# Kernel optimization log

Hardware: AMD Instinct MI355X
Metric: run time of the kernel (lower is better)

## Reference

```python
import jax, jax.numpy as jnp
import numpy as np
import math

B, C, D, H, W = 8, 128, 64, 32, 32
SHRINK = C // 2  # 64
EPS = 1e-5


def setup_inputs() -> dict:
    key = jax.random.key(0)
    ks = jax.random.split(key, 7)
    x = jax.random.normal(ks[0], (B, C, D, H, W), dtype=jnp.float32)
    # 1x1x1 Conv3d weights collapse to [out_ch, in_ch] matrices (no bias)
    def kaiming(k, shape):
        fan_in = shape[1]
        return jax.random.normal(k, shape, dtype=jnp.float32) * np.float32(math.sqrt(2.0 / fan_in))
    Wk = kaiming(ks[1], (SHRINK, C))
    Wq = kaiming(ks[2], (SHRINK, C))
    Wv = kaiming(ks[3], (SHRINK, C))
    Wo = kaiming(ks[4], (C, SHRINK))
    gamma = jnp.ones((C,), dtype=jnp.float32)
    beta = jnp.zeros((C,), dtype=jnp.float32)
    return {"x": x, "Wk": Wk, "Wq": Wq, "Wv": Wv, "Wo": Wo, "gamma": gamma, "beta": beta}


def reference(x, Wk, Wq, Wv, Wo, gamma, beta):
    b, c, d, h, w = x.shape
    s = Wk.shape[0]
    # BatchNorm3d (training mode: batch statistics over B, D, H, W)
    mean = jnp.mean(x, axis=(0, 2, 3, 4), keepdims=True)
    var = jnp.var(x, axis=(0, 2, 3, 4), keepdims=True)
    xn = (x - mean) * jax.lax.rsqrt(var + EPS)
    xn = xn * gamma[None, :, None, None, None] + beta[None, :, None, None, None]
    # fold spatial into batch: [B*H*W, C, D]
    xr = jnp.transpose(xn, (0, 3, 4, 1, 2)).reshape(b * h * w, c, d)
    k = jnp.einsum('sc,ncd->nsd', Wk, xr)  # [N, S, D]
    q = jnp.einsum('sc,ncd->nsd', Wq, xr)
    v = jnp.einsum('sc,ncd->nsd', Wv, xr)
    scores = jnp.einsum('nsi,nsj->nij', k, q) / jnp.float32(math.sqrt(s))  # [N, D, D]
    a = jax.nn.softmax(scores, axis=1)  # softmax over key-time axis (dim=1)
    attn = jnp.einsum('nsi,nij->nsj', v, a)  # [N, S, D]
    attn = attn.reshape(b, h, w, s, d)
    out = jnp.einsum('os,bhwsd->bodhw', Wo, attn)  # 1x1x1 conv out proj
    return x + out
```

## Files before the change

kernel.cpp:

```cpp
#include <hip/hip_runtime.h>

typedef __attribute__((ext_vector_type(8))) short short8;
typedef __attribute__((ext_vector_type(4))) float f32x4;
typedef unsigned short u16;
typedef unsigned int u32;

#define CNT_PER_C (8*64*32*32)

#define WS_PART  0
#define WS_SCALE 8192
#define WS_SHIFT 8704
#define WS_BIAS  9216
#define WS_WKQV  10240
#define WS_WO    59392
#define WS_OUTP  131072

__device__ __forceinline__ u16 f2bf(float f){
  u32 u = __builtin_bit_cast(u32, f);
  u32 r = u + 0x7FFFu + ((u >> 16) & 1u);
  return (u16)(r >> 16);
}
__device__ __forceinline__ float bf2f(u16 h){
  u32 u = ((u32)h) << 16;
  return __builtin_bit_cast(float, u);
}
__device__ __forceinline__ u32 pk2(float a, float b){
  return (u32)f2bf(a) | ((u32)f2bf(b) << 16);
}

__global__ void k_zero(float* part){
  part[blockIdx.x*256 + threadIdx.x] = 0.f;
}

__global__ __launch_bounds__(256) void k_stats_t(const float* __restrict__ x,
                                                 u16* __restrict__ x_t,
                                                 float* __restrict__ part){
  __shared__ u16 lm[32*512];
  __shared__ float cs[256];
  int t = threadIdx.x;
  cs[t] = 0.f;
  int bid = blockIdx.x;
  int bh = bid>>3, dq = bid&7;
  int b = bh>>5, h = bh&31;
  int d0 = dq*8, n0 = bh*32;
  int s = t>>3, q = t&7;
  float sA=0.f,qA=0.f, sB=0.f,qB=0.f, sC=0.f,qC=0.f, sD=0.f,qD=0.f;
  __syncthreads();
#pragma unroll
  for (int h2=0; h2<2; h2++){
    int w4 = q*4;
#pragma unroll
    for (int i=0;i<16;i++){
      int rowpos = i*32 + s;
      int cl = rowpos & 63, dd = rowpos >> 6;
      int c = h2*64 + cl;
      float4 v = *(const float4*)(x + ((size_t)((b*128 + c)*64 + d0 + dd))*1024 + h*32 + w4);
      float lsum = v.x+v.y+v.z+v.w;
      float lsq  = v.x*v.x+v.y*v.y+v.z*v.z+v.w*v.w;
      if (h2==0){ if ((i&1)==0){ sA+=lsum; qA+=lsq; } else { sB+=lsum; qB+=lsq; } }
      else      { if ((i&1)==0){ sC+=lsum; qC+=lsq; } else { sD+=lsum; qD+=lsq; } }
      lm[(w4+0)*512 + (rowpos ^ ((w4+0)&28))] = f2bf(v.x);
      lm[(w4+1)*512 + (rowpos ^ ((w4+1)&28))] = f2bf(v.y);
      lm[(w4+2)*512 + (rowpos ^ ((w4+2)&28))] = f2bf(v.z);
      lm[(w4+3)*512 + (rowpos ^ ((w4+3)&28))] = f2bf(v.w);
    }
    __syncthreads();
    {
      int n = s, oct = q;
      int oq = oct ^ ((n>>3)&3);
      bool swp = (n & 4) != 0;
#pragma unroll
      for (int m=0;m<8;m++){
        uint4 raw = *(const uint4*)&lm[n*512 + m*64 + oq*8];
        if (swp){ u32 tx=raw.x, ty=raw.y; raw.x=raw.z; raw.y=raw.w; raw.z=tx; raw.w=ty; }
        *(uint4*)(x_t + (size_t)(n0+n)*8192 + (size_t)(d0+m)*128 + h2*64 + oct*8) = raw;
      }
    }
    __syncthreads();
  }
  atomicAdd(&cs[(s    )*2+0], sA); atomicAdd(&cs[(s    )*2+1], qA);
  atomicAdd(&cs[(s+32 )*2+0], sB); atomicAdd(&cs[(s+32 )*2+1], qB);
  atomicAdd(&cs[(s+64 )*2+0], sC); atomicAdd(&cs[(s+64 )*2+1], qC);
  atomicAdd(&cs[(s+96 )*2+0], sD); atomicAdd(&cs[(s+96 )*2+1], qD);
  __syncthreads();
  atomicAdd(&part[(bid&7)*256 + t], cs[t]);
}

__global__ void k_stats2(const float* part, const float* gamma, const float* beta,
                         float* scale, float* shift){
  int c = threadIdx.x;
  float S=0.f, S2=0.f;
  for (int i=0;i<8;i++){ S += part[i*256 + c*2]; S2 += part[i*256 + c*2 + 1]; }
  float inv = 1.0f/(float)CNT_PER_C;
  float mean = S*inv;
  float var  = S2*inv - mean*mean;
  float rstd = rsqrtf(var + 1e-5f);
  float sc = gamma[c]*rstd;
  scale[c] = sc; shift[c] = beta[c] - mean*sc;
}

__global__ __launch_bounds__(256) void k_wprep(const float* wk, const float* wq, const float* wv,
                                               const float* wo, const float* scale,
                                               const float* shift, u16* wkqv_bf, u16* wo_bf,
                                               float* bias){
  int t = threadIdx.x;
  if (t < 192){
    const float* src = (t<64) ? (wk + t*128) : (t<128) ? (wq + (t-64)*128) : (wv + (t-128)*128);
    float bsum = 0.f;
    for (int c=0;c<128;c++){
      float w = src[c];
      bsum += w*shift[c];
      wkqv_bf[t*128+c] = f2bf(w*scale[c]);
    }
    bias[t] = bsum;
  }
  for (int j=t; j<8192; j+=256) wo_bf[j] = f2bf(wo[j]);
}

__global__ __launch_bounds__(256, 2) void k_attn(const u16* __restrict__ x_t,
                                                 const u16* __restrict__ wkqv,
                                                 const u16* __restrict__ wo,
                                                 const float* __restrict__ bias,
                                                 u16* __restrict__ out_pre){
  __shared__ alignas(16) char smb[65536];
  const int t = threadIdx.x, lane = t & 63, wid = t >> 6;
  const int lr = lane & 15, lk = lane >> 4;
  const int n = blockIdx.x*4 + wid;
  char* slot = smb + wid*16384;
  char* lo = slot;
  char* hi = slot + 8192;
  const u16* xg = x_t + (size_t)n*8192;

  short8 xbf[4][4];
#pragma unroll
  for (int ct=0; ct<4; ct++)
#pragma unroll
    for (int ks=0; ks<4; ks++)
      xbf[ct][ks] = *(const short8*)(xg + (ct*16+lr)*128 + ks*32 + lk*8);

#pragma unroll
  for (int mt=0; mt<4; mt++){
    short8 af[4];
#pragma unroll
    for (int ks=0; ks<4; ks++)
      af[ks] = *(const short8*)(wkqv + (size_t)(mt*16 + lr)*128 + ks*32 + lk*8);
    float4 bk4 = *(const float4*)(bias + mt*16 + lk*4);
#pragma unroll
    for (int ct=0; ct<4; ct++){
      f32x4 a = (f32x4){0.f,0.f,0.f,0.f};
#pragma unroll
      for (int ks=0; ks<4; ks++)
        a = __builtin_amdgcn_mfma_f32_16x16x32_bf16(af[ks], xbf[ct][ks], a, 0,0,0);
      a[0]+=bk4.x; a[1]+=bk4.y; a[2]+=bk4.z; a[3]+=bk4.w;
      int d = ct*16 + lr;
      *(uint2*)(lo + d*128 + ((mt*32 + lk*8) ^ ((d&7)<<4))) =
        (uint2){pk2(a[0],a[1]), pk2(a[2],a[3])};
    }
  }
#pragma unroll
  for (int mt=0; mt<4; mt++){
    short8 af[4];
#pragma unroll
    for (int ks=0; ks<4; ks++)
      af[ks] = *(const short8*)(wkqv + (size_t)((mt+4)*16 + lr)*128 + ks*32 + lk*8);
    float4 bq4 = *(const float4*)(bias + 64 + mt*16 + lk*4);
#pragma unroll
    for (int ct=0; ct<4; ct++){
      f32x4 a = (f32x4){0.f,0.f,0.f,0.f};
#pragma unroll
      for (int ks=0; ks<4; ks++)
        a = __builtin_amdgcn_mfma_f32_16x16x32_bf16(af[ks], xbf[ct][ks], a, 0,0,0);
      a[0]+=bq4.x; a[1]+=bq4.y; a[2]+=bq4.z; a[3]+=bq4.w;
      int d = ct*16 + lr;
      *(uint2*)(hi + d*128 + ((mt*32 + lk*8) ^ ((d&7)<<4))) =
        (uint2){pk2(a[0],a[1]), pk2(a[2],a[3])};
    }
  }
  f32x4 vacc[4][4];
#pragma unroll
  for (int mt=0; mt<4; mt++){
    short8 af[4];
#pragma unroll
    for (int ks=0; ks<4; ks++)
      af[ks] = *(const short8*)(wkqv + (size_t)((mt+8)*16 + lr)*128 + ks*32 + lk*8);
    float4 bv4 = *(const float4*)(bias + 128 + mt*16 + lk*4);
#pragma unroll
    for (int ct=0; ct<4; ct++) vacc[mt][ct] = (f32x4){0.f,0.f,0.f,0.f};
#pragma unroll
    for (int ct=0; ct<4; ct++){
#pragma unroll
      for (int ks=0; ks<4; ks++)
        vacc[mt][ct] = __builtin_amdgcn_mfma_f32_16x16x32_bf16(af[ks], xbf[ct][ks], vacc[mt][ct], 0,0,0);
      vacc[mt][ct][0]+=bv4.x; vacc[mt][ct][1]+=bv4.y;
      vacc[mt][ct][2]+=bv4.z; vacc[mt][ct][3]+=bv4.w;
    }
  }

  short8 ka[4][2];
#pragma unroll
  for (int it=0; it<4; it++)
#pragma unroll
    for (int ks2=0; ks2<2; ks2++){
      int i = it*16 + lr;
      ka[it][ks2] = *(const short8*)(lo + i*128 + ((ks2*64 + lk*16) ^ ((i&7)<<4)));
    }
#pragma unroll
  for (int m4=0; m4<4; m4++)
#pragma unroll
    for (int ct=0; ct<4; ct++)
#pragma unroll
      for (int e=0; e<4; e++){
        int sp = m4*16 + lk*4 + e, i = ct*16 + lr;
        *(u16*)(lo + sp*128 + ((i*2) ^ ((sp&7)<<4))) = f2bf(vacc[m4][ct][e]);
      }
  short8 qb[4][2];
#pragma unroll
  for (int jt=0; jt<4; jt++)
#pragma unroll
    for (int ks2=0; ks2<2; ks2++){
      int j = jt*16 + lr;
      qb[jt][ks2] = *(const short8*)(hi + j*128 + ((ks2*64 + lk*16) ^ ((j&7)<<4)));
    }
  f32x4 sc4[4][4];
#pragma unroll
  for (int it=0; it<4; it++)
#pragma unroll
    for (int jt=0; jt<4; jt++) sc4[it][jt] = (f32x4){0.f,0.f,0.f,0.f};
#pragma unroll
  for (int it=0; it<4; it++)
#pragma unroll
    for (int jt=0; jt<4; jt++)
#pragma unroll
      for (int ks2=0; ks2<2; ks2++)
        sc4[it][jt] = __builtin_amdgcn_mfma_f32_16x16x32_bf16(ka[it][ks2], qb[jt][ks2], sc4[it][jt], 0,0,0);

#pragma unroll
  for (int jt=0; jt<4; jt++){
    float m = -1e30f;
#pragma unroll
    for (int it=0; it<4; it++)
#pragma unroll
      for (int e=0; e<4; e++) m = fmaxf(m, sc4[it][jt][e]);
    m = fmaxf(m, __shfl_xor(m, 16, 64));
    m = fmaxf(m, __shfl_xor(m, 32, 64));
    float ssum = 0.f;
#pragma unroll
    for (int it=0; it<4; it++)
#pragma unroll
      for (int e=0; e<4; e++){
        float p = __expf((sc4[it][jt][e] - m) * 0.125f);
        sc4[it][jt][e] = p; ssum += p;
      }
    ssum += __shfl_xor(ssum, 16, 64);
    ssum += __shfl_xor(ssum, 32, 64);
    float inv = 1.0f / ssum;
    int j = jt*16 + lr;
#pragma unroll
    for (int it=0; it<4; it++){
      *(uint2*)(hi + j*128 + ((it*32 + lk*8) ^ ((j&7)<<4))) =
        (uint2){pk2(sc4[it][jt][0]*inv, sc4[it][jt][1]*inv),
                pk2(sc4[it][jt][2]*inv, sc4[it][jt][3]*inv)};
    }
  }

  short8 va[4][2], ab[4][2];
#pragma unroll
  for (int st=0; st<4; st++)
#pragma unroll
    for (int ks2=0; ks2<2; ks2++){
      int s2 = st*16 + lr;
      va[st][ks2] = *(const short8*)(lo + s2*128 + ((ks2*64 + lk*16) ^ ((s2&7)<<4)));
    }
#pragma unroll
  for (int jt=0; jt<4; jt++)
#pragma unroll
    for (int ks2=0; ks2<2; ks2++){
      int j = jt*16 + lr;
      ab[jt][ks2] = *(const short8*)(hi + j*128 + ((ks2*64 + lk*16) ^ ((j&7)<<4)));
    }
  f32x4 at4[4][4];
#pragma unroll
  for (int st=0; st<4; st++)
#pragma unroll
    for (int jt=0; jt<4; jt++) at4[st][jt] = (f32x4){0.f,0.f,0.f,0.f};
#pragma unroll
  for (int st=0; st<4; st++)
#pragma unroll
    for (int jt=0; jt<4; jt++)
#pragma unroll
      for (int ks2=0; ks2<2; ks2++)
        at4[st][jt] = __builtin_amdgcn_mfma_f32_16x16x32_bf16(va[st][ks2], ab[jt][ks2], at4[st][jt], 0,0,0);
#pragma unroll
  for (int st=0; st<4; st++)
#pragma unroll
    for (int jt=0; jt<4; jt++){
      int d = jt*16 + lr;
      *(uint2*)(lo + d*128 + ((st*32 + lk*8) ^ ((d&7)<<4))) =
        (uint2){pk2(at4[st][jt][0], at4[st][jt][1]), pk2(at4[st][jt][2], at4[st][jt][3])};
    }

  short8 tb[4][2];
#pragma unroll
  for (int dt=0; dt<4; dt++)
#pragma unroll
    for (int ks2=0; ks2<2; ks2++){
      int d = dt*16 + lr;
      tb[dt][ks2] = *(const short8*)(lo + d*128 + ((ks2*64 + lk*16) ^ ((d&7)<<4)));
    }
#pragma unroll
  for (int mt=0; mt<8; mt++){
    short8 wa[2];
#pragma unroll
    for (int ks2=0; ks2<2; ks2++)
      wa[ks2] = *(const short8*)(wo + (size_t)(mt*16 + lr)*64 + ks2*32 + lk*8);
    f32x4 oa[4];
#pragma unroll
    for (int dt=0; dt<4; dt++) oa[dt] = (f32x4){0.f,0.f,0.f,0.f};
#pragma unroll
    for (int dt=0; dt<4; dt++)
#pragma unroll
      for (int ks2=0; ks2<2; ks2++)
        oa[dt] = __builtin_amdgcn_mfma_f32_16x16x32_bf16(wa[ks2], tb[dt][ks2], oa[dt], 0,0,0);
#pragma unroll
    for (int dt=0; dt<4; dt++){
      ushort4 xv = *(const ushort4*)(xg + (size_t)(dt*16+lr)*128 + mt*16 + lk*4);
      oa[dt][0] += bf2f(xv.x);
      oa[dt][1] += bf2f(xv.y);
      oa[dt][2] += bf2f(xv.z);
      oa[dt][3] += bf2f(xv.w);
    }
#pragma unroll
    for (int dt=0; dt<4; dt++)
#pragma unroll
      for (int e=0; e<4; e++){
        int cc = mt*16 + lk*4 + e, d = dt*16 + lr;
        *(u16*)(slot + cc*128 + ((d*2) ^ ((cc&7)<<4))) = f2bf(oa[dt][e]);
      }
  }

  u16* og = out_pre + (size_t)n*8192;
#pragma unroll
  for (int r=0;r<16;r++){
    int j = r*64 + lane;
    int cc = j>>3, o = j&7;
    uint4 v = *(const uint4*)(slot + cc*128 + ((o*16) ^ ((cc&7)<<4)));
    *(uint4*)(og + j*8) = v;
  }
}

__global__ __launch_bounds__(256) void k_merge(const u16* out_pre, float* out){
  __shared__ u16 lm[32*512];
  int t = threadIdx.x;
  int bid = blockIdx.x;
  int bh = bid>>2, cq = bid&3;
  int b = bh>>5, h = bh&31;
  int n0 = bh*32;
  int cbase = cq*32;
  int s = t>>3, q = t&7;
  for (int cc=0; cc<4; cc++){
    int cb = cbase + cc*8;
    {
      int n = s;
      int oq = q ^ ((n>>3)&3);
      bool swp = (n & 4) != 0;
#pragma unroll
      for (int i=0;i<8;i++){
        uint4 raw = *(const uint4*)(out_pre + (size_t)(n0+n)*8192 + (cb+i)*64 + q*8);
        if (swp){ u32 tx=raw.x, ty=raw.y; raw.x=raw.z; raw.y=raw.w; raw.z=tx; raw.w=ty; }
        *(uint4*)&lm[n*512 + i*64 + oq*8] = raw;
      }
    }
    __syncthreads();
    {
      int w4 = q*4;
#pragma unroll
      for (int g=0; g<16; g++){
        int row = g*32 + s;
        int ci = row>>6, d = row&63;
        size_t gi = ((size_t)((b*128 + cb + ci)*64 + d))*1024 + h*32 + w4;
        float4 ov;
        ov.x = bf2f(lm[(w4+0)*512 + (row ^ ((w4+0)&28))]);
        ov.y = bf2f(lm[(w4+1)*512 + (row ^ ((w4+1)&28))]);
        ov.z = bf2f(lm[(w4+2)*512 + (row ^ ((w4+2)&28))]);
        ov.w = bf2f(lm[(w4+3)*512 + (row ^ ((w4+3)&28))]);
        *(float4*)(out + gi) = ov;
      }
    }
    __syncthreads();
  }
}

extern "C" void kernel_launch(void* const* d_in, const int* in_sizes, int n_in,
                              void* d_out, int out_size, void* d_ws, size_t ws_size,
                              hipStream_t stream){
  const float* x     = (const float*)d_in[0];
  const float* Wk    = (const float*)d_in[1];
  const float* Wq    = (const float*)d_in[2];
  const float* Wv    = (const float*)d_in[3];
  const float* Wo    = (const float*)d_in[4];
  const float* gamma = (const float*)d_in[5];
  const float* beta  = (const float*)d_in[6];
  float* out = (float*)d_out;
  char* ws = (char*)d_ws;

  float* part  = (float*)(ws + WS_PART);
  float* scale = (float*)(ws + WS_SCALE);
  float* shift = (float*)(ws + WS_SHIFT);
  float* bias  = (float*)(ws + WS_BIAS);
  u16* wkqv  = (u16*)(ws + WS_WKQV);
  u16* wo_bf = (u16*)(ws + WS_WO);
  u16* outp  = (u16*)(ws + WS_OUTP);
  u16* x_t   = (u16*)d_out;

  k_zero   <<<8,    256, 0, stream>>>(part);
  k_stats_t<<<2048, 256, 0, stream>>>(x, x_t, part);
  k_stats2 <<<1,    128, 0, stream>>>(part, gamma, beta, scale, shift);
  k_wprep  <<<1,    256, 0, stream>>>(Wk, Wq, Wv, Wo, scale, shift, wkqv, wo_bf, bias);
  k_attn   <<<2048, 256, 0, stream>>>(x_t, wkqv, wo_bf, bias, outp);
  k_merge  <<<1024, 256, 0, stream>>>(outp, out);
}
```

Baseline: 328.0 us.

## Fuse output transpose into attention kernel and merge stats/weight-prep kernels

The attention kernel now writes fp32 output directly to the final NCDHW layout. Blocks are remapped so that each block's four waves cover four consecutive w positions of the same (b,h), which lets each thread store a float4 along w. This removes the bf16 out_pre intermediate and the separate k_merge transpose kernel, saving a full round trip through global memory. k_stats2 and k_wprep are also merged into one kernel that keeps scale and shift in shared memory, cutting one launch. The stores are now 16-byte chunks strided by 4 KB rather than coalesced rows, and x_t moves from the output buffer into the workspace.

After: 407.5 us. +24.2%, slower.

```diff
diff --git a/kernel.cpp b/kernel.cpp
--- a/kernel.cpp
+++ b/kernel.cpp
@@ -8,12 +8,10 @@
 #define CNT_PER_C (8*64*32*32)
 
 #define WS_PART  0
-#define WS_SCALE 8192
-#define WS_SHIFT 8704
 #define WS_BIAS  9216
 #define WS_WKQV  10240
 #define WS_WO    59392
-#define WS_OUTP  131072
+#define WS_XT    131072
 
 __device__ __forceinline__ u16 f2bf(float f){
   u32 u = __builtin_bit_cast(u32, f);
@@ -86,46 +84,50 @@
   atomicAdd(&part[(bid&7)*256 + t], cs[t]);
 }
 
-__global__ void k_stats2(const float* part, const float* gamma, const float* beta,
-                         float* scale, float* shift){
-  int c = threadIdx.x;
-  float S=0.f, S2=0.f;
-  for (int i=0;i<8;i++){ S += part[i*256 + c*2]; S2 += part[i*256 + c*2 + 1]; }
-  float inv = 1.0f/(float)CNT_PER_C;
-  float mean = S*inv;
-  float var  = S2*inv - mean*mean;
-  float rstd = rsqrtf(var + 1e-5f);
-  float sc = gamma[c]*rstd;
-  scale[c] = sc; shift[c] = beta[c] - mean*sc;
-}
-
-__global__ __launch_bounds__(256) void k_wprep(const float* wk, const float* wq, const float* wv,
-                                               const float* wo, const float* scale,
-                                               const float* shift, u16* wkqv_bf, u16* wo_bf,
-                                               float* bias){
+__global__ __launch_bounds__(256) void k_finalize(const float* part, const float* gamma,
+                                                  const float* beta, const float* wk,
+                                                  const float* wq, const float* wv,
+                                                  const float* wo, u16* wkqv_bf, u16* wo_bf,
+                                                  float* bias){
+  __shared__ float lsc[128], lsh[128];
   int t = threadIdx.x;
+  if (t < 128){
+    float S=0.f, S2=0.f;
+    for (int i=0;i<8;i++){ S += part[i*256 + t*2]; S2 += part[i*256 + t*2 + 1]; }
+    float inv = 1.0f/(float)CNT_PER_C;
+    float mean = S*inv;
+    float var  = S2*inv - mean*mean;
+    float rstd = rsqrtf(var + 1e-5f);
+    float sc = gamma[t]*rstd;
+    lsc[t] = sc; lsh[t] = beta[t] - mean*sc;
+  }
+  __syncthreads();
   if (t < 192){
     const float* src = (t<64) ? (wk + t*128) : (t<128) ? (wq + (t-64)*128) : (wv + (t-128)*128);
     float bsum = 0.f;
     for (int c=0;c<128;c++){
       float w = src[c];
-      bsum += w*shift[c];
-      wkqv_bf[t*128+c] = f2bf(w*scale[c]);
+      bsum += w*lsh[c];
+      wkqv_bf[t*128+c] = f2bf(w*lsc[c]);
     }
     bias[t] = bsum;
   }
   for (int j=t; j<8192; j+=256) wo_bf[j] = f2bf(wo[j]);
 }
 
-__global__ __launch_bounds__(256, 2) void k_attn(const u16* __restrict__ x_t,
-                                                 const u16* __restrict__ wkqv,
-                                                 const u16* __restrict__ wo,
-                                                 const float* __restrict__ bias,
-                                                 u16* __restrict__ out_pre){
+__global__ __launch_bounds__(256, 2) void k_attn_w(const u16* __restrict__ x_t,
+                                                   const u16* __restrict__ wkqv,
+                                                   const u16* __restrict__ wo,
+                                                   const float* __restrict__ bias,
+                                                   float* __restrict__ out){
   __shared__ alignas(16) char smb[65536];
   const int t = threadIdx.x, lane = t & 63, wid = t >> 6;
   const int lr = lane & 15, lk = lane >> 4;
-  const int n = blockIdx.x*4 + wid;
+  const int p = blockIdx.x;
+  const int bh = (p & 7)*32 + (p >> 6);
+  const int wg = (p >> 3) & 7;
+  const int b = bh >> 5, h = bh & 31;
+  const int n = bh*32 + wg*4 + wid;
   char* slot = smb + wid*16384;
   char* lo = slot;
   char* hi = slot + 8192;
@@ -248,8 +250,8 @@
     for (int it=0; it<4; it++)
 #pragma unroll
       for (int e=0; e<4; e++){
-        float p = __expf((sc4[it][jt][e] - m) * 0.125f);
-        sc4[it][jt][e] = p; ssum += p;
+        float pp = __expf((sc4[it][jt][e] - m) * 0.125f);
+        sc4[it][jt][e] = pp; ssum += pp;
       }
     ssum += __shfl_xor(ssum, 16, 64);
     ssum += __shfl_xor(ssum, 32, 64);
@@ -338,55 +340,19 @@
       }
   }
 
-  u16* og = out_pre + (size_t)n*8192;
-#pragma unroll
-  for (int r=0;r<16;r++){
-    int j = r*64 + lane;
-    int cc = j>>3, o = j&7;
-    uint4 v = *(const uint4*)(slot + cc*128 + ((o*16) ^ ((cc&7)<<4)));
-    *(uint4*)(og + j*8) = v;
-  }
-}
-
-__global__ __launch_bounds__(256) void k_merge(const u16* out_pre, float* out){
-  __shared__ u16 lm[32*512];
-  int t = threadIdx.x;
-  int bid = blockIdx.x;
-  int bh = bid>>2, cq = bid&3;
-  int b = bh>>5, h = bh&31;
-  int n0 = bh*32;
-  int cbase = cq*32;
-  int s = t>>3, q = t&7;
-  for (int cc=0; cc<4; cc++){
-    int cb = cbase + cc*8;
-    {
-      int n = s;
-      int oq = q ^ ((n>>3)&3);
-      bool swp = (n & 4) != 0;
-#pragma unroll
-      for (int i=0;i<8;i++){
-        uint4 raw = *(const uint4*)(out_pre + (size_t)(n0+n)*8192 + (cb+i)*64 + q*8);
-        if (swp){ u32 tx=raw.x, ty=raw.y; raw.x=raw.z; raw.y=raw.w; raw.z=tx; raw.w=ty; }
-        *(uint4*)&lm[n*512 + i*64 + oq*8] = raw;
-      }
-    }
-    __syncthreads();
-    {
-      int w4 = q*4;
-#pragma unroll
-      for (int g=0; g<16; g++){
-        int row = g*32 + s;
-        int ci = row>>6, d = row&63;
-        size_t gi = ((size_t)((b*128 + cb + ci)*64 + d))*1024 + h*32 + w4;
-        float4 ov;
-        ov.x = bf2f(lm[(w4+0)*512 + (row ^ ((w4+0)&28))]);
-        ov.y = bf2f(lm[(w4+1)*512 + (row ^ ((w4+1)&28))]);
-        ov.z = bf2f(lm[(w4+2)*512 + (row ^ ((w4+2)&28))]);
-        ov.w = bf2f(lm[(w4+3)*512 + (row ^ ((w4+3)&28))]);
-        *(float4*)(out + gi) = ov;
-      }
-    }
-    __syncthreads();
+  __syncthreads();
+  const int w0 = wg*4;
+#pragma unroll
+  for (int i=0; i<32; i++){
+    int c = i*4 + wid;
+    int d = lane;
+    int off = c*128 + ((d*2) ^ ((c&7)<<4));
+    float4 ov;
+    ov.x = bf2f(*(const u16*)(smb +     0 + off));
+    ov.y = bf2f(*(const u16*)(smb + 16384 + off));
+    ov.z = bf2f(*(const u16*)(smb + 32768 + off));
+    ov.w = bf2f(*(const u16*)(smb + 49152 + off));
+    *(float4*)(out + ((size_t)((b*128+c)*64) + d)*1024 + h*32 + w0) = ov;
   }
 }
 
@@ -404,18 +370,13 @@
   char* ws = (char*)d_ws;
 
   float* part  = (float*)(ws + WS_PART);
-  float* scale = (float*)(ws + WS_SCALE);
-  float* shift = (float*)(ws + WS_SHIFT);
   float* bias  = (float*)(ws + WS_BIAS);
   u16* wkqv  = (u16*)(ws + WS_WKQV);
   u16* wo_bf = (u16*)(ws + WS_WO);
-  u16* outp  = (u16*)(ws + WS_OUTP);
-  u16* x_t   = (u16*)d_out;
-
-  k_zero   <<<8,    256, 0, stream>>>(part);
-  k_stats_t<<<2048, 256, 0, stream>>>(x, x_t, part);
-  k_stats2 <<<1,    128, 0, stream>>>(part, gamma, beta, scale, shift);
-  k_wprep  <<<1,    256, 0, stream>>>(Wk, Wq, Wv, Wo, scale, shift, wkqv, wo_bf, bias);
-  k_attn   <<<2048, 256, 0, stream>>>(x_t, wkqv, wo_bf, bias, outp);
-  k_merge  <<<1024, 256, 0, stream>>>(outp, out);
-}
+  u16* x_t   = (u16*)(ws + WS_XT);
+
+  k_zero    <<<8,    256, 0, stream>>>(part);
+  k_stats_t <<<2048, 256, 0, stream>>>(x, x_t, part);
+  k_finalize<<<1,    256, 0, stream>>>(part, gamma, beta, Wk, Wq, Wv, Wo, wkqv, wo_bf, bias);
+  k_attn_w  <<<2048, 256, 0, stream>>>(x_t, wkqv, wo_bf, bias, out);
+}
```

## Halve attention LDS footprint and merge stats finalize into weight prep kernel

Applied to the files above, without the earlier changes.

The attention kernel now uses one 8 KB LDS slot per wave instead of 16 KB. K and Q fragments are read into registers right after each is written, and the output projection is written out in two channel halves so the smaller slot can be reused throughout. This halves shared memory per block, which should let more blocks fit per CU, at the cost of more live registers and reordered LDS reuse. Separately, the BN stats finalize kernel is fused into the weight-prep kernel to remove one tiny launch.

Measured after the change: 322.5 us. Within noise of the previous version (-1.7%).

```diff
diff --git a/kernel.cpp b/kernel.cpp
--- a/kernel.cpp
+++ b/kernel.cpp
@@ -8,8 +8,6 @@
 #define CNT_PER_C (8*64*32*32)
 
 #define WS_PART  0
-#define WS_SCALE 8192
-#define WS_SHIFT 8704
 #define WS_BIAS  9216
 #define WS_WKQV  10240
 #define WS_WO    59392
@@ -86,31 +84,31 @@
   atomicAdd(&part[(bid&7)*256 + t], cs[t]);
 }
 
-__global__ void k_stats2(const float* part, const float* gamma, const float* beta,
-                         float* scale, float* shift){
-  int c = threadIdx.x;
-  float S=0.f, S2=0.f;
-  for (int i=0;i<8;i++){ S += part[i*256 + c*2]; S2 += part[i*256 + c*2 + 1]; }
-  float inv = 1.0f/(float)CNT_PER_C;
-  float mean = S*inv;
-  float var  = S2*inv - mean*mean;
-  float rstd = rsqrtf(var + 1e-5f);
-  float sc = gamma[c]*rstd;
-  scale[c] = sc; shift[c] = beta[c] - mean*sc;
-}
-
-__global__ __launch_bounds__(256) void k_wprep(const float* wk, const float* wq, const float* wv,
-                                               const float* wo, const float* scale,
-                                               const float* shift, u16* wkqv_bf, u16* wo_bf,
-                                               float* bias){
+__global__ __launch_bounds__(256) void k_finalize(const float* part, const float* gamma,
+                                                  const float* beta, const float* wk,
+                                                  const float* wq, const float* wv,
+                                                  const float* wo, u16* wkqv_bf, u16* wo_bf,
+                                                  float* bias){
+  __shared__ float lsc[128], lsh[128];
   int t = threadIdx.x;
+  if (t < 128){
+    float S=0.f, S2=0.f;
+    for (int i=0;i<8;i++){ S += part[i*256 + t*2]; S2 += part[i*256 + t*2 + 1]; }
+    float inv = 1.0f/(float)CNT_PER_C;
+    float mean = S*inv;
+    float var  = S2*inv - mean*mean;
+    float rstd = rsqrtf(var + 1e-5f);
+    float sc = gamma[t]*rstd;
+    lsc[t] = sc; lsh[t] = beta[t] - mean*sc;
+  }
+  __syncthreads();
   if (t < 192){
     const float* src = (t<64) ? (wk + t*128) : (t<128) ? (wq + (t-64)*128) : (wv + (t-128)*128);
     float bsum = 0.f;
     for (int c=0;c<128;c++){
       float w = src[c];
-      bsum += w*shift[c];
-      wkqv_bf[t*128+c] = f2bf(w*scale[c]);
+      bsum += w*lsh[c];
+      wkqv_bf[t*128+c] = f2bf(w*lsc[c]);
     }
     bias[t] = bsum;
   }
@@ -122,13 +120,11 @@
                                                  const u16* __restrict__ wo,
                                                  const float* __restrict__ bias,
                                                  u16* __restrict__ out_pre){
-  __shared__ alignas(16) char smb[65536];
+  __shared__ alignas(16) char smb[32768];
   const int t = threadIdx.x, lane = t & 63, wid = t >> 6;
   const int lr = lane & 15, lk = lane >> 4;
   const int n = blockIdx.x*4 + wid;
-  char* slot = smb + wid*16384;
-  char* lo = slot;
-  char* hi = slot + 8192;
+  char* slot = smb + wid*8192;
   const u16* xg = x_t + (size_t)n*8192;
 
   short8 xbf[4][4];
@@ -153,10 +149,19 @@
         a = __builtin_amdgcn_mfma_f32_16x16x32_bf16(af[ks], xbf[ct][ks], a, 0,0,0);
       a[0]+=bk4.x; a[1]+=bk4.y; a[2]+=bk4.z; a[3]+=bk4.w;
       int d = ct*16 + lr;
-      *(uint2*)(lo + d*128 + ((mt*32 + lk*8) ^ ((d&7)<<4))) =
+      *(uint2*)(slot + d*128 + ((mt*32 + lk*8) ^ ((d&7)<<4))) =
         (uint2){pk2(a[0],a[1]), pk2(a[2],a[3])};
     }
   }
+  short8 ka[4][2];
+#pragma unroll
+  for (int it=0; it<4; it++)
+#pragma unroll
+    for (int ks2=0; ks2<2; ks2++){
+      int i = it*16 + lr;
+      ka[it][ks2] = *(const short8*)(slot + i*128 + ((ks2*64 + lk*16) ^ ((i&7)<<4)));
+    }
+
 #pragma unroll
   for (int mt=0; mt<4; mt++){
     short8 af[4];
@@ -172,10 +177,19 @@
         a = __builtin_amdgcn_mfma_f32_16x16x32_bf16(af[ks], xbf[ct][ks], a, 0,0,0);
       a[0]+=bq4.x; a[1]+=bq4.y; a[2]+=bq4.z; a[3]+=bq4.w;
       int d = ct*16 + lr;
-      *(uint2*)(hi + d*128 + ((mt*32 + lk*8) ^ ((d&7)<<4))) =
+      *(uint2*)(slot + d*128 + ((mt*32 + lk*8) ^ ((d&7)<<4))) =
         (uint2){pk2(a[0],a[1]), pk2(a[2],a[3])};
     }
   }
+  short8 qb[4][2];
+#pragma unroll
+  for (int jt=0; jt<4; jt++)
+#pragma unroll
+    for (int ks2=0; ks2<2; ks2++){
+      int j = jt*16 + lr;
+      qb[jt][ks2] = *(const short8*)(slot + j*128 + ((ks2*64 + lk*16) ^ ((j&7)<<4)));
+    }
+
   f32x4 vacc[4][4];
 #pragma unroll
   for (int mt=0; mt<4; mt++){
@@ -195,15 +209,6 @@
       vacc[mt][ct][2]+=bv4.z; vacc[mt][ct][3]+=bv4.w;
     }
   }
-
-  short8 ka[4][2];
-#pragma unroll
-  for (int it=0; it<4; it++)
-#pragma unroll
-    for (int ks2=0; ks2<2; ks2++){
-      int i = it*16 + lr;
-      ka[it][ks2] = *(const short8*)(lo + i*128 + ((ks2*64 + lk*16) ^ ((i&7)<<4)));
-    }
 #pragma unroll
   for (int m4=0; m4<4; m4++)
 #pragma unroll
@@ -211,16 +216,9 @@
 #pragma unroll
       for (int e=0; e<4; e++){
         int sp = m4*16 + lk*4 + e, i = ct*16 + lr;
-        *(u16*)(lo + sp*128 + ((i*2) ^ ((sp&7)<<4))) = f2bf(vacc[m4][ct][e]);
-      }
-  short8 qb[4][2];
-#pragma unroll
-  for (int jt=0; jt<4; jt++)
-#pragma unroll
-    for (int ks2=0; ks2<2; ks2++){
-      int j = jt*16 + lr;
-      qb[jt][ks2] = *(const short8*)(hi + j*128 + ((ks2*64 + lk*16) ^ ((j&7)<<4)));
-    }
+        *(u16*)(slot + sp*128 + ((i*2) ^ ((sp&7)<<4))) = f2bf(vacc[m4][ct][e]);
+      }
+
   f32x4 sc4[4][4];
 #pragma unroll
   for (int it=0; it<4; it++)
@@ -254,30 +252,39 @@
     ssum += __shfl_xor(ssum, 16, 64);
     ssum += __shfl_xor(ssum, 32, 64);
     float inv = 1.0f / ssum;
-    int j = jt*16 + lr;
-#pragma unroll
-    for (int it=0; it<4; it++){
-      *(uint2*)(hi + j*128 + ((it*32 + lk*8) ^ ((j&7)<<4))) =
-        (uint2){pk2(sc4[it][jt][0]*inv, sc4[it][jt][1]*inv),
-                pk2(sc4[it][jt][2]*inv, sc4[it][jt][3]*inv)};
-    }
-  }
-
-  short8 va[4][2], ab[4][2];
+#pragma unroll
+    for (int it=0; it<4; it++)
+#pragma unroll
+      for (int e=0; e<4; e++) sc4[it][jt][e] *= inv;
+  }
+
+  short8 va[4][2];
 #pragma unroll
   for (int st=0; st<4; st++)
 #pragma unroll
     for (int ks2=0; ks2<2; ks2++){
       int s2 = st*16 + lr;
-      va[st][ks2] = *(const short8*)(lo + s2*128 + ((ks2*64 + lk*16) ^ ((s2&7)<<4)));
-    }
+      va[st][ks2] = *(const short8*)(slot + s2*128 + ((ks2*64 + lk*16) ^ ((s2&7)<<4)));
+    }
+#pragma unroll
+  for (int jt=0; jt<4; jt++){
+    int j = jt*16 + lr;
+#pragma unroll
+    for (int it=0; it<4; it++){
+      *(uint2*)(slot + j*128 + ((it*32 + lk*8) ^ ((j&7)<<4))) =
+        (uint2){pk2(sc4[it][jt][0], sc4[it][jt][1]),
+                pk2(sc4[it][jt][2], sc4[it][jt][3])};
+    }
+  }
+  short8 ab[4][2];
 #pragma unroll
   for (int jt=0; jt<4; jt++)
 #pragma unroll
     for (int ks2=0; ks2<2; ks2++){
       int j = jt*16 + lr;
-      ab[jt][ks2] = *(const short8*)(hi + j*128 + ((ks2*64 + lk*16) ^ ((j&7)<<4)));
-    }
+      ab[jt][ks2] = *(const short8*)(slot + j*128 + ((ks2*64 + lk*16) ^ ((j&7)<<4)));
+    }
+
   f32x4 at4[4][4];
 #pragma unroll
   for (int st=0; st<4; st++)
@@ -295,56 +302,58 @@
 #pragma unroll
     for (int jt=0; jt<4; jt++){
       int d = jt*16 + lr;
-      *(uint2*)(lo + d*128 + ((st*32 + lk*8) ^ ((d&7)<<4))) =
+      *(uint2*)(slot + d*128 + ((st*32 + lk*8) ^ ((d&7)<<4))) =
         (uint2){pk2(at4[st][jt][0], at4[st][jt][1]), pk2(at4[st][jt][2], at4[st][jt][3])};
     }
-
   short8 tb[4][2];
 #pragma unroll
   for (int dt=0; dt<4; dt++)
 #pragma unroll
     for (int ks2=0; ks2<2; ks2++){
       int d = dt*16 + lr;
-      tb[dt][ks2] = *(const short8*)(lo + d*128 + ((ks2*64 + lk*16) ^ ((d&7)<<4)));
-    }
-#pragma unroll
-  for (int mt=0; mt<8; mt++){
-    short8 wa[2];
-#pragma unroll
-    for (int ks2=0; ks2<2; ks2++)
-      wa[ks2] = *(const short8*)(wo + (size_t)(mt*16 + lr)*64 + ks2*32 + lk*8);
-    f32x4 oa[4];
-#pragma unroll
-    for (int dt=0; dt<4; dt++) oa[dt] = (f32x4){0.f,0.f,0.f,0.f};
-#pragma unroll
-    for (int dt=0; dt<4; dt++)
+      tb[dt][ks2] = *(const short8*)(slot + d*128 + ((ks2*64 + lk*16) ^ ((d&7)<<4)));
+    }
+
+  u16* og = out_pre + (size_t)n*8192;
+#pragma unroll
+  for (int hf=0; hf<2; hf++){
+#pragma unroll
+    for (int mt=0; mt<4; mt++){
+      short8 wa[2];
 #pragma unroll
       for (int ks2=0; ks2<2; ks2++)
-        oa[dt] = __builtin_amdgcn_mfma_f32_16x16x32_bf16(wa[ks2], tb[dt][ks2], oa[dt], 0,0,0);
-#pragma unroll
-    for (int dt=0; dt<4; dt++){
-      ushort4 xv = *(const ushort4*)(xg + (size_t)(dt*16+lr)*128 + mt*16 + lk*4);
-      oa[dt][0] += bf2f(xv.x);
-      oa[dt][1] += bf2f(xv.y);
-      oa[dt][2] += bf2f(xv.z);
-      oa[dt][3] += bf2f(xv.w);
-    }
-#pragma unroll
-    for (int dt=0; dt<4; dt++)
-#pragma unroll
-      for (int e=0; e<4; e++){
-        int cc = mt*16 + lk*4 + e, d = dt*16 + lr;
-        *(u16*)(slot + cc*128 + ((d*2) ^ ((cc&7)<<4))) = f2bf(oa[dt][e]);
-      }
-  }
-
-  u16* og = out_pre + (size_t)n*8192;
-#pragma unroll
-  for (int r=0;r<16;r++){
-    int j = r*64 + lane;
-    int cc = j>>3, o = j&7;
-    uint4 v = *(const uint4*)(slot + cc*128 + ((o*16) ^ ((cc&7)<<4)));
-    *(uint4*)(og + j*8) = v;
+        wa[ks2] = *(const short8*)(wo + (size_t)((hf*4+mt)*16 + lr)*64 + ks2*32 + lk*8);
+      f32x4 oa[4];
+#pragma unroll
+      for (int dt=0; dt<4; dt++) oa[dt] = (f32x4){0.f,0.f,0.f,0.f};
+#pragma unroll
+      for (int dt=0; dt<4; dt++)
+#pragma unroll
+        for (int ks2=0; ks2<2; ks2++)
+          oa[dt] = __builtin_amdgcn_mfma_f32_16x16x32_bf16(wa[ks2], tb[dt][ks2], oa[dt], 0,0,0);
+#pragma unroll
+      for (int dt=0; dt<4; dt++){
+        ushort4 xv = *(const ushort4*)(xg + (size_t)(dt*16+lr)*128 + hf*64 + mt*16 + lk*4);
+        oa[dt][0] += bf2f(xv.x);
+        oa[dt][1] += bf2f(xv.y);
+        oa[dt][2] += bf2f(xv.z);
+        oa[dt][3] += bf2f(xv.w);
+      }
+#pragma unroll
+      for (int dt=0; dt<4; dt++)
+#pragma unroll
+        for (int e=0; e<4; e++){
+          int cl = mt*16 + lk*4 + e, d = dt*16 + lr;
+          *(u16*)(slot + cl*128 + ((d*2) ^ ((cl&7)<<4))) = f2bf(oa[dt][e]);
+        }
+    }
+#pragma unroll
+    for (int r=0;r<8;r++){
+      int j = r*64 + lane;
+      int cc = j>>3, o = j&7;
+      uint4 v = *(const uint4*)(slot + cc*128 + ((o*16) ^ ((cc&7)<<4)));
+      *(uint4*)(og + hf*4096 + j*8) = v;
+    }
   }
 }
 
@@ -404,18 +413,15 @@
   char* ws = (char*)d_ws;
 
   float* part  = (float*)(ws + WS_PART);
-  float* scale = (float*)(ws + WS_SCALE);
-  float* shift = (float*)(ws + WS_SHIFT);
   float* bias  = (float*)(ws + WS_BIAS);
   u16* wkqv  = (u16*)(ws + WS_WKQV);
   u16* wo_bf = (u16*)(ws + WS_WO);
   u16* outp  = (u16*)(ws + WS_OUTP);
   u16* x_t   = (u16*)d_out;
 
-  k_zero   <<<8,    256, 0, stream>>>(part);
-  k_stats_t<<<2048, 256, 0, stream>>>(x, x_t, part);
-  k_stats2 <<<1,    128, 0, stream>>>(part, gamma, beta, scale, shift);
-  k_wprep  <<<1,    256, 0, stream>>>(Wk, Wq, Wv, Wo, scale, shift, wkqv, wo_bf, bias);
-  k_attn   <<<2048, 256, 0, stream>>>(x_t, wkqv, wo_bf, bias, outp);
-  k_merge  <<<1024, 256, 0, stream>>>(outp, out);
-}
+  k_zero    <<<8,    256, 0, stream>>>(part);
+  k_stats_t <<<2048, 256, 0, stream>>>(x, x_t, part);
+  k_finalize<<<1,    256, 0, stream>>>(part, gamma, beta, Wk, Wq, Wv, Wo, wkqv, wo_bf, bias);
+  k_attn    <<<2048, 256, 0, stream>>>(x_t, wkqv, wo_bf, bias, outp);
+  k_merge   <<<1024, 256, 0, stream>>>(outp, out);
+}
```
